# Kernel tuning notes

Hardware: AMD Instinct MI355X
Metric: run time of the kernel (lower is better)

The kernel has to match this reference:

```python
import jax, jax.numpy as jnp
import numpy as np
from jax import lax

NEG = -1e30  # effective -inf in fp32, safe under logaddexp
BLANK = 0


def setup_inputs() -> dict:
    key = jax.random.key(0)
    k1, k2, k3, k4 = jax.random.split(key, 4)
    B, T, V, S = 64, 2000, 128, 100
    logits = jax.random.normal(k1, (B, T, V), dtype=jnp.float32)
    targets = jax.random.randint(k2, (B, S), 1, V)  # exclude blank=0
    logits_lengths = jax.random.randint(k3, (B,), T // 2, T + 1)
    targets_lengths = jax.random.randint(k4, (B,), S // 2, S + 1)
    return {"logits": logits, "targets": targets,
            "logits_lengths": logits_lengths, "targets_lengths": targets_lengths}


def _ctc_neg_log_lik(log_probs, targets, in_lens, tgt_lens):
    # log_probs: [B, T, V] log-softmax; targets: [B, S]; lengths: [B]
    B, T, V = log_probs.shape
    S = targets.shape[1]
    L = 2 * S + 1  # extended label seq: blank, l1, blank, l2, ..., blank
    ext = jnp.full((B, L), BLANK, dtype=targets.dtype).at[:, 1::2].set(targets)
    # per-time emission log-prob of each extended-label slot: [B, T, L]
    lp_ext = jnp.take_along_axis(log_probs, ext[:, None, :], axis=2)
    # skip transition s-2 -> s allowed iff ext[s] != blank and ext[s] != ext[s-2]
    ext_m2 = jnp.pad(ext[:, :-2], ((0, 0), (2, 0)), constant_values=BLANK)
    skip = (ext != BLANK) & (ext != ext_m2)  # [B, L]

    alpha0 = jnp.full((B, L), NEG, dtype=log_probs.dtype)
    alpha0 = alpha0.at[:, 0].set(lp_ext[:, 0, 0])
    alpha0 = alpha0.at[:, 1].set(jnp.where(tgt_lens > 0, lp_ext[:, 0, 1], NEG))

    def step(alpha, xs):
        lp_t, t = xs  # lp_t: [B, L]
        a1 = jnp.pad(alpha[:, :-1], ((0, 0), (1, 0)), constant_values=NEG)
        a2 = jnp.where(skip,
                       jnp.pad(alpha[:, :-2], ((0, 0), (2, 0)), constant_values=NEG),
                       NEG)
        new = jnp.logaddexp(jnp.logaddexp(alpha, a1), a2) + lp_t
        # freeze alpha once past each utterance's length
        alpha = jnp.where((t < in_lens)[:, None], new, alpha)
        return alpha, None

    xs = (jnp.moveaxis(lp_ext, 1, 0)[1:], jnp.arange(1, T))
    alpha_T, _ = lax.scan(step, alpha0, xs)

    idx = 2 * tgt_lens  # final blank slot
    last_blank = jnp.take_along_axis(alpha_T, idx[:, None], axis=1)[:, 0]
    last_label = jnp.take_along_axis(alpha_T, jnp.maximum(idx - 1, 0)[:, None], axis=1)[:, 0]
    last_label = jnp.where(tgt_lens > 0, last_label, NEG)
    return -jnp.logaddexp(last_blank, last_label)  # [B]


def reference(logits, targets, logits_lengths, targets_lengths):
    log_probs = jax.nn.log_softmax(logits, axis=2)
    loss = _ctc_neg_log_lik(log_probs, targets, logits_lengths, targets_lengths)
    return loss.sum()  # reduce=True
```

## Files before the change

### kernel.cpp

```cpp
#include <hip/hip_runtime.h>
#include <hip/hip_fp16.h>
#include <math.h>

#define BB 64
#define TT 2000
#define VV 128
#define SS 100
#define NP 1000
#define PRB 448
#define LN2D 0.6931471805599453

__device__ __forceinline__ float wave_sum_f32(float v) {
    int t;
    t = __builtin_amdgcn_update_dpp(0, __float_as_int(v), 0x111, 0xF, 0xF, true);  v += __int_as_float(t);
    t = __builtin_amdgcn_update_dpp(0, __float_as_int(v), 0x112, 0xF, 0xF, true);  v += __int_as_float(t);
    t = __builtin_amdgcn_update_dpp(0, __float_as_int(v), 0x114, 0xF, 0xF, true);  v += __int_as_float(t);
    t = __builtin_amdgcn_update_dpp(0, __float_as_int(v), 0x118, 0xF, 0xF, true);  v += __int_as_float(t);
    t = __builtin_amdgcn_update_dpp(0, __float_as_int(v), 0x142, 0xA, 0xF, false); v += __int_as_float(t);
    t = __builtin_amdgcn_update_dpp(0, __float_as_int(v), 0x143, 0xC, 0xF, false); v += __int_as_float(t);
    return __int_as_float(__builtin_amdgcn_readlane(__float_as_int(v), 63));
}

__device__ __forceinline__ void half_sums_f32(float v, float* sA, float* sB) {
    int t;
    t = __builtin_amdgcn_update_dpp(0, __float_as_int(v), 0x111, 0xF, 0xF, true);  v += __int_as_float(t);
    t = __builtin_amdgcn_update_dpp(0, __float_as_int(v), 0x112, 0xF, 0xF, true);  v += __int_as_float(t);
    t = __builtin_amdgcn_update_dpp(0, __float_as_int(v), 0x114, 0xF, 0xF, true);  v += __int_as_float(t);
    t = __builtin_amdgcn_update_dpp(0, __float_as_int(v), 0x118, 0xF, 0xF, true);  v += __int_as_float(t);
    t = __builtin_amdgcn_update_dpp(0, __float_as_int(v), 0x142, 0xA, 0xF, false); v += __int_as_float(t);
    *sA = __int_as_float(__builtin_amdgcn_readlane(__float_as_int(v), 31));
    *sB = __int_as_float(__builtin_amdgcn_readlane(__float_as_int(v), 63));
}

__global__ __launch_bounds__(256) void ctc_k1(
    const float* __restrict__ logits, const int* __restrict__ targets,
    ushort* __restrict__ pe2, float* __restrict__ logSb)
{
    const int wv = threadIdx.x >> 6, lane = threadIdx.x & 63;
    const int gp = blockIdx.x * 4 + wv;
    const int b = gp / NP, p = gp - b * NP;
    const int tA = 2 * p + 1, tB = 2 * p + 2;
    const bool vB = (tB < TT);

    const int trow = (lane < 32) ? tA : (vB ? tB : tA);
    float4 x4 = reinterpret_cast<const float4*>(logits + ((size_t)b * TT + trow) * VV)[lane & 31];

    float e0 = __expf(x4.x), e1 = __expf(x4.y);
    float e2 = __expf(x4.z), e3 = __expf(x4.w);
    float sa, sb;
    half_sums_f32((e0 + e1) + (e2 + e3), &sa, &sb);

    __shared__ float sm[4][2][VV];
    {
        float4 ev; ev.x = e0; ev.y = e1; ev.z = e2; ev.w = e3;
        *reinterpret_cast<float4*>(&sm[wv][lane >> 5][(lane & 31) * 4]) = ev;
    }

    int tg0 = 0, tg1 = 0;
    if (lane < 50) {
        int2 tg = reinterpret_cast<const int2*>(targets)[b * (SS / 2) + lane];
        tg0 = tg.x; tg1 = tg.y;
    }
    const float qiA = 1.0f / sm[wv][0][0];
    const float qiB = 1.0f / sm[wv][1][0];
    float q1a = 0.f, q3a = 0.f, q1b = 0.f, q3b = 0.f;
    if (lane < 50) {
        q1a = fminf(sm[wv][0][tg0] * qiA, 65504.f);
        q3a = fminf(sm[wv][0][tg1] * qiA, 65504.f);
        if (vB) {
            q1b = fminf(sm[wv][1][tg0] * qiB, 65504.f);
            q3b = fminf(sm[wv][1][tg1] * qiB, 65504.f);
        }
    }
    if (lane < 56) {
        ushort4 w;
        w.x = __half_as_ushort(__float2half_rn(q1a));
        w.y = __half_as_ushort(__float2half_rn(q3a));
        w.z = __half_as_ushort(__float2half_rn(q1b));
        w.w = __half_as_ushort(__float2half_rn(q3b));
        *reinterpret_cast<ushort4*>((char*)pe2 + ((size_t)b * NP + p) * PRB + lane * 8) = w;
    }
    if (lane == 0) {
        float xB0 = __int_as_float(__builtin_amdgcn_readlane(__float_as_int(x4.x), 32));
        logSb[b * TT + tA] = __logf(sa) - x4.x;
        if (vB) logSb[b * TT + tB] = __logf(sb) - xB0;
    }
}

union H4 { uint2 u; __half h[4]; };

__device__ __forceinline__ double dpp_shr1_f64(double x) {
    long long bl = __double_as_longlong(x);
    int lo = (int)bl, hi = (int)(bl >> 32);
    lo = __builtin_amdgcn_update_dpp(0, lo, 0x138, 0xF, 0xF, true);
    hi = __builtin_amdgcn_update_dpp(0, hi, 0x138, 0xF, 0xF, true);
    return __longlong_as_double((long long)(((unsigned long long)(unsigned)hi << 32) | (unsigned)lo));
}

__device__ __forceinline__ double dpp_shl1_f64(double x) {
    long long bl = __double_as_longlong(x);
    int lo = (int)bl, hi = (int)(bl >> 32);
    lo = __builtin_amdgcn_update_dpp(0, lo, 0x130, 0xF, 0xF, true);
    hi = __builtin_amdgcn_update_dpp(0, hi, 0x130, 0xF, 0xF, true);
    return __longlong_as_double((long long)(((unsigned long long)(unsigned)hi << 32) | (unsigned)lo));
}

__device__ __forceinline__ int wave_max_i32(int v) {
    int t;
    t = __builtin_amdgcn_update_dpp(0, v, 0x111, 0xF, 0xF, true); v = v > t ? v : t;
    t = __builtin_amdgcn_update_dpp(0, v, 0x112, 0xF, 0xF, true); v = v > t ? v : t;
    t = __builtin_amdgcn_update_dpp(0, v, 0x114, 0xF, 0xF, true); v = v > t ? v : t;
    t = __builtin_amdgcn_update_dpp(0, v, 0x118, 0xF, 0xF, true); v = v > t ? v : t;
    t = __builtin_amdgcn_update_dpp(v, v, 0x142, 0xA, 0xF, false); v = v > t ? v : t;
    t = __builtin_amdgcn_update_dpp(v, v, 0x143, 0xC, 0xF, false); v = v > t ? v : t;
    return __builtin_amdgcn_readlane(v, 63);
}

#define FSTEP(Q1, Q3) do {                                   \
    double am1 = dpp_shr1_f64(a3);                           \
    double t23 = a2 + a3;                                    \
    double n3 = fma(sk3, a1, t23) * (Q3);                    \
    double t01 = a0 + a1;                                    \
    double n1 = fma(sk1, am1, t01) * (Q1);                   \
    double n0 = a0 + am1;                                    \
    double n2 = a1 + a2;                                     \
    a0 = n0; a1 = n1; a2 = n2; a3 = n3;                      \
} while (0)

#define BSTEP(Q1, Q3) do {                                   \
    double bp0 = dpp_shl1_f64(a0);                           \
    double bp1 = dpp_shl1_f64(a1);                           \
    double t12 = a1 + a2;                                    \
    double c1 = fma(sk3, a3, t12) * (Q1);                    \
    double c0 = a0 + a1;                                     \
    double t30 = a3 + bp0;                                   \
    double c3 = fma(skB, bp1, t30) * (Q3);                   \
    double c2 = a2 + a3;                                     \
    a0 = c0; a1 = c1; a2 = c2; a3 = c3;                      \
} while (0)

#define RENORM() do {                                        \
    int h0 = (int)(__double_as_longlong(a0) >> 32);          \
    int h1 = (int)(__double_as_longlong(a1) >> 32);          \
    int h2 = (int)(__double_as_longlong(a2) >> 32);          \
    int h3 = (int)(__double_as_longlong(a3) >> 32);          \
    int m01 = h0 > h1 ? h0 : h1;                             \
    int m23 = h2 > h3 ? h2 : h3;                             \
    int mm  = wave_max_i32(m01 > m23 ? m01 : m23);           \
    int ex  = (mm >> 20) & 0x7FF;                            \
    int exc = ex > 0 ? ex : 1;                               \
    double f = __longlong_as_double((long long)(2046 - exc) << 52); \
    a0 *= f; a1 *= f; a2 *= f; a3 *= f;                      \
    Epow += exc - 1023;                                      \
} while (0)

#define CVT4(H, Q1A, Q3A, Q1B, Q3B) do {                     \
    Q1A = (double)__half2float((H).h[0]);                    \
    Q3A = (double)__half2float((H).h[1]);                    \
    Q1B = (double)__half2float((H).h[2]);                    \
    Q3B = (double)__half2float((H).h[3]); } while (0)

__global__ __launch_bounds__(128) void ctc_k2(
    const float* __restrict__ logits, const ushort* __restrict__ pe2,
    const float* __restrict__ logSb, const int* __restrict__ targets,
    const int* __restrict__ in_lens, const int* __restrict__ tgt_lens,
    float* __restrict__ out)
{
    const int b    = blockIdx.x;
    const int tid  = threadIdx.x;
    const int wv   = tid >> 6;
    const int lane = tid & 63;
    const int n    = in_lens[b];
    const int tl   = tgt_lens[b];

    const int P  = (13 * (n - 2)) / 50;
    const int pL = (n - 2) >> 1;

    __shared__ double SA[256];
    __shared__ double SC[256];
    __shared__ double sred[2];
    __shared__ int    sE[2];

    int tg0 = 0, tg1 = 0, tgm1 = 0, tg2 = 0;
    if (lane < 50) {
        int2 tg = reinterpret_cast<const int2*>(targets)[b * (SS / 2) + lane];
        tg0 = tg.x; tg1 = tg.y;
    }
    if (lane >= 1 && lane <= 50) tgm1 = targets[b * SS + 2 * lane - 1];
    if (lane <= 48) tg2 = targets[b * SS + 2 * lane + 2];
    const double sk1 = (tg0 != tgm1) ? 1.0 : 0.0;
    const double sk3 = (tg1 != tg0)  ? 1.0 : 0.0;
    const double skB = (tg2 != tg1)  ? 1.0 : 0.0;

    const int cl = (lane < 51) ? lane : 50;
    const char* PBbase = (const char*)pe2 + (size_t)b * NP * PRB + (size_t)cl * 8;

    double a0 = 0.0, a1 = 0.0, a2 = 0.0, a3 = 0.0;
    int Epow = 0;
    double lsb0 = 0.0;
    uint2 buf[16];

    if (wv == 0) {
        float2 x0 = reinterpret_cast<const float2*>(logits + (size_t)b * TT * VV)[lane];
        float e00 = __expf(x0.x), e01 = __expf(x0.y);
        float s0v = wave_sum_f32(e00 + e01);
        float qb0 = __shfl(e00, 0);
        int ext1 = targets[b * SS];
        float qn = __shfl((ext1 & 1) ? e01 : e00, ext1 >> 1);
        if (lane == 0) {
            a0 = 1.0;
            if (tl > 0) a1 = (double)qn / (double)qb0;
            lsb0 = (double)__logf(s0v) - (double)x0.x;
        }

        #pragma unroll
        for (int d = 0; d < 16; ++d)
            buf[d] = *reinterpret_cast<const uint2*>(PBbase + (size_t)d * PRB);
        const char* Pc = PBbase + (size_t)16 * PRB;
        double c1A, c3A, c1B, c3B, n1A, n3A, n1B, n3B;
        { H4 h0; h0.u = buf[0]; CVT4(h0, c1A, c3A, c1B, c3B); }
        const int nfull = P >> 4, rem = P & 15;
        for (int c = 0; c < nfull; ++c) {
            #pragma unroll
            for (int d = 0; d < 16; ++d) {
                H4 hn; hn.u = buf[(d + 1) & 15];
                buf[d] = *reinterpret_cast<const uint2*>(Pc + (size_t)d * PRB);
                CVT4(hn, n1A, n3A, n1B, n3B);
                FSTEP(c1A, c3A);
                FSTEP(c1B, c3B);
                c1A = n1A; c3A = n3A; c1B = n1B; c3B = n3B;
            }
            RENORM();
            Pc += (size_t)16 * PRB;
        }
        #pragma unroll
        for (int d = 0; d < 16; ++d) {
            if (d < rem) {
                H4 h; h.u = buf[d];
                double q1A, q3A, q1B, q3B; CVT4(h, q1A, q3A, q1B, q3B);
                FSTEP(q1A, q3A);
                FSTEP(q1B, q3B);
            }
        }
        RENORM();
        SA[4 * lane + 0] = a0; SA[4 * lane + 1] = a1;
        SA[4 * lane + 2] = a2; SA[4 * lane + 3] = a3;
        if (lane == 0) sE[0] = Epow;
    } else {
        H4 hi; hi.u = *reinterpret_cast<const uint2*>(PBbase + (size_t)pL * PRB);
        const bool nOdd = (n & 1);
        double q1i = (double)__half2float(nOdd ? hi.h[2] : hi.h[0]);
        double q3i = (double)__half2float(nOdd ? hi.h[3] : hi.h[1]);
        const int s2 = 2 * tl, s1 = 2 * tl - 1;
        a0 = (4 * lane     == s2) ? 1.0 : 0.0;
        a1 = (4 * lane + 1 == s1) ? q1i : 0.0;
        a2 = (4 * lane + 2 == s2) ? 1.0 : 0.0;
        a3 = (4 * lane + 3 == s1) ? q3i : 0.0;
        if (nOdd) {
            double q1 = (double)__half2float(hi.h[0]);
            double q3 = (double)__half2float(hi.h[1]);
            BSTEP(q1, q3);
        }

        const int NB = pL - P;
        #pragma unroll
        for (int d = 0; d < 16; ++d)
            buf[d] = *reinterpret_cast<const uint2*>(PBbase + (size_t)(pL - 1 - d) * PRB);
        const char* Pc = PBbase + (size_t)(pL - 1 - 16) * PRB;
        double c1A, c3A, c1B, c3B, n1A, n3A, n1B, n3B;
        { H4 h0; h0.u = buf[0]; CVT4(h0, c1A, c3A, c1B, c3B); }
        const int nfull = NB >> 4, rem = NB & 15;
        for (int c = 0; c < nfull; ++c) {
            #pragma unroll
            for (int d = 0; d < 16; ++d) {
                H4 hn; hn.u = buf[(d + 1) & 15];
                buf[d] = *reinterpret_cast<const uint2*>(Pc - (size_t)d * PRB);
                CVT4(hn, n1A, n3A, n1B, n3B);
                BSTEP(c1B, c3B);
                BSTEP(c1A, c3A);
                c1A = n1A; c3A = n3A; c1B = n1B; c3B = n3B;
            }
            RENORM();
            Pc -= (size_t)16 * PRB;
        }
        #pragma unroll
        for (int d = 0; d < 16; ++d) {
            if (d < rem) {
                H4 h; h.u = buf[d];
                double q1A, q3A, q1B, q3B; CVT4(h, q1A, q3A, q1B, q3B);
                BSTEP(q1B, q3B);
                BSTEP(q1A, q3A);
            }
        }
        RENORM();
        {
            double bp0 = dpp_shl1_f64(a0);
            double bp1 = dpp_shl1_f64(a1);
            double c0 = a0 + a1;
            double c1 = fma(sk3, a3, a1 + a2);
            double c2 = a2 + a3;
            double c3 = fma(skB, bp1, a3 + bp0);
            SC[4 * lane + 0] = c0; SC[4 * lane + 1] = c1;
            SC[4 * lane + 2] = c2; SC[4 * lane + 3] = c3;
        }
        if (lane == 0) sE[1] = Epow;
    }

    double cb = 0.0;
    for (int t = 1 + tid; t < n; t += 128) cb += (double)logSb[b * TT + t];
    #pragma unroll
    for (int off = 32; off; off >>= 1) cb += __shfl_xor(cb, off);
    if (lane == 0) sred[wv] = cb;

    __syncthreads();

    if (wv == 0) {
        double d0 = SA[4 * lane + 0] * SC[4 * lane + 0]
                  + SA[4 * lane + 1] * SC[4 * lane + 1]
                  + SA[4 * lane + 2] * SC[4 * lane + 2]
                  + SA[4 * lane + 3] * SC[4 * lane + 3];
        #pragma unroll
        for (int off = 32; off; off >>= 1) d0 += __shfl_xor(d0, off);
        if (lane == 0) {
            double dot = d0;
            int extraE = 0;
            long long bits = __double_as_longlong(dot);
            int be = (int)((bits >> 52) & 0x7FF);
            if (be == 0) {
                dot *= 0x1.0p+512;
                bits = __double_as_longlong(dot);
                be = (int)((bits >> 52) & 0x7FF);
                extraE = -512;
            }
            double mant = __longlong_as_double((bits & 0xFFFFFFFFFFFFFLL) | 0x3FF0000000000000LL);
            double logdot = ((double)(be - 1023 + extraE + sE[0] + sE[1])) * LN2D
                          + (double)__logf((float)mant);
            double loss = (sred[0] + sred[1] + lsb0) - logdot;
            atomicAdd(out, (float)loss);
        }
    }
}

extern "C" void kernel_launch(void* const* d_in, const int* in_sizes, int n_in,
                              void* d_out, int out_size, void* d_ws, size_t ws_size,
                              hipStream_t stream)
{
    const float* logits  = (const float*)d_in[0];
    const int* targets   = (const int*)d_in[1];
    const int* in_lens   = (const int*)d_in[2];
    const int* tgt_lens  = (const int*)d_in[3];
    float* out = (float*)d_out;

    ushort* pe2 = (ushort*)d_ws;
    float* logSb = (float*)((char*)d_ws + (size_t)BB * NP * PRB);

    hipMemsetAsync(d_out, 0, sizeof(float), stream);
    ctc_k1<<<BB * NP / 4, 256, 0, stream>>>(logits, targets, pe2, logSb);
    ctc_k2<<<BB, 128, 0, stream>>>(logits, pe2, logSb, targets, in_lens, tgt_lens, out);
}
```

Before: 65.87 us.

## Interleave forward and backward CTC recursions in one wave, skip padded steps

The second kernel now runs the forward and backward alpha/beta recursions interleaved inside a single 64-lane wave instead of on two separate waves. This gives each wave two independent dependency chains to hide FP64 latency and removes the shared-memory exchange and block barrier. The split point moves from about 26% forward to an even half. The first kernel now returns early for time pairs past each utterance's length and zeroes the output itself, which replaces the memset launch. The risk is that the single wave's serial chain gets longer, and that zeroing the output from block 0 depends on kernel ordering.

New measurement: 105.7 us. +60.4%, slower.

```diff
diff --git a/kernel.cpp b/kernel.cpp
--- a/kernel.cpp
+++ b/kernel.cpp
@@ -34,11 +34,15 @@
 
 __global__ __launch_bounds__(256) void ctc_k1(
     const float* __restrict__ logits, const int* __restrict__ targets,
-    ushort* __restrict__ pe2, float* __restrict__ logSb)
+    const int* __restrict__ in_lens, ushort* __restrict__ pe2,
+    float* __restrict__ logSb, float* __restrict__ out)
 {
+    if (blockIdx.x == 0 && threadIdx.x == 0) out[0] = 0.f;
     const int wv = threadIdx.x >> 6, lane = threadIdx.x & 63;
     const int gp = blockIdx.x * 4 + wv;
     const int b = gp / NP, p = gp - b * NP;
+    const int n = in_lens[b];
+    if (p > ((n - 2) >> 1)) return;
     const int tA = 2 * p + 1, tB = 2 * p + 2;
     const bool vB = (tB < TT);
 
@@ -128,30 +132,30 @@
 } while (0)
 
 #define BSTEP(Q1, Q3) do {                                   \
-    double bp0 = dpp_shl1_f64(a0);                           \
-    double bp1 = dpp_shl1_f64(a1);                           \
-    double t12 = a1 + a2;                                    \
-    double c1 = fma(sk3, a3, t12) * (Q1);                    \
-    double c0 = a0 + a1;                                     \
-    double t30 = a3 + bp0;                                   \
+    double bp0 = dpp_shl1_f64(b0);                           \
+    double bp1 = dpp_shl1_f64(b1);                           \
+    double t12 = b1 + b2;                                    \
+    double c1 = fma(sk3, b3, t12) * (Q1);                    \
+    double c0 = b0 + b1;                                     \
+    double t30 = b3 + bp0;                                   \
     double c3 = fma(skB, bp1, t30) * (Q3);                   \
-    double c2 = a2 + a3;                                     \
-    a0 = c0; a1 = c1; a2 = c2; a3 = c3;                      \
+    double c2 = b2 + b3;                                     \
+    b0 = c0; b1 = c1; b2 = c2; b3 = c3;                      \
 } while (0)
 
-#define RENORM() do {                                        \
-    int h0 = (int)(__double_as_longlong(a0) >> 32);          \
-    int h1 = (int)(__double_as_longlong(a1) >> 32);          \
-    int h2 = (int)(__double_as_longlong(a2) >> 32);          \
-    int h3 = (int)(__double_as_longlong(a3) >> 32);          \
+#define RENORM4(X0, X1, X2, X3, EP) do {                     \
+    int h0 = (int)(__double_as_longlong(X0) >> 32);          \
+    int h1 = (int)(__double_as_longlong(X1) >> 32);          \
+    int h2 = (int)(__double_as_longlong(X2) >> 32);          \
+    int h3 = (int)(__double_as_longlong(X3) >> 32);          \
     int m01 = h0 > h1 ? h0 : h1;                             \
     int m23 = h2 > h3 ? h2 : h3;                             \
     int mm  = wave_max_i32(m01 > m23 ? m01 : m23);           \
     int ex  = (mm >> 20) & 0x7FF;                            \
     int exc = ex > 0 ? ex : 1;                               \
     double f = __longlong_as_double((long long)(2046 - exc) << 52); \
-    a0 *= f; a1 *= f; a2 *= f; a3 *= f;                      \
-    Epow += exc - 1023;                                      \
+    X0 *= f; X1 *= f; X2 *= f; X3 *= f;                      \
+    EP += exc - 1023;                                        \
 } while (0)
 
 #define CVT4(H, Q1A, Q3A, Q1B, Q3B) do {                     \
@@ -160,26 +164,20 @@
     Q1B = (double)__half2float((H).h[2]);                    \
     Q3B = (double)__half2float((H).h[3]); } while (0)
 
-__global__ __launch_bounds__(128) void ctc_k2(
+__global__ __launch_bounds__(64) void ctc_k2(
     const float* __restrict__ logits, const ushort* __restrict__ pe2,
     const float* __restrict__ logSb, const int* __restrict__ targets,
     const int* __restrict__ in_lens, const int* __restrict__ tgt_lens,
     float* __restrict__ out)
 {
     const int b    = blockIdx.x;
-    const int tid  = threadIdx.x;
-    const int wv   = tid >> 6;
-    const int lane = tid & 63;
+    const int lane = threadIdx.x;
     const int n    = in_lens[b];
     const int tl   = tgt_lens[b];
 
-    const int P  = (13 * (n - 2)) / 50;
     const int pL = (n - 2) >> 1;
-
-    __shared__ double SA[256];
-    __shared__ double SC[256];
-    __shared__ double sred[2];
-    __shared__ int    sE[2];
+    const int P  = (pL + 1) >> 1;
+    const int NB = pL - P;
 
     int tg0 = 0, tg1 = 0, tgm1 = 0, tg2 = 0;
     if (lane < 50) {
@@ -196,11 +194,8 @@
     const char* PBbase = (const char*)pe2 + (size_t)b * NP * PRB + (size_t)cl * 8;
 
     double a0 = 0.0, a1 = 0.0, a2 = 0.0, a3 = 0.0;
-    int Epow = 0;
     double lsb0 = 0.0;
-    uint2 buf[16];
-
-    if (wv == 0) {
+    {
         float2 x0 = reinterpret_cast<const float2*>(logits + (size_t)b * TT * VV)[lane];
         float e00 = __expf(x0.x), e01 = __expf(x0.y);
         float s0v = wave_sum_f32(e00 + e01);
@@ -212,132 +207,111 @@
             if (tl > 0) a1 = (double)qn / (double)qb0;
             lsb0 = (double)__logf(s0v) - (double)x0.x;
         }
-
-        #pragma unroll
-        for (int d = 0; d < 16; ++d)
-            buf[d] = *reinterpret_cast<const uint2*>(PBbase + (size_t)d * PRB);
-        const char* Pc = PBbase + (size_t)16 * PRB;
-        double c1A, c3A, c1B, c3B, n1A, n3A, n1B, n3B;
-        { H4 h0; h0.u = buf[0]; CVT4(h0, c1A, c3A, c1B, c3B); }
-        const int nfull = P >> 4, rem = P & 15;
-        for (int c = 0; c < nfull; ++c) {
-            #pragma unroll
-            for (int d = 0; d < 16; ++d) {
-                H4 hn; hn.u = buf[(d + 1) & 15];
-                buf[d] = *reinterpret_cast<const uint2*>(Pc + (size_t)d * PRB);
-                CVT4(hn, n1A, n3A, n1B, n3B);
-                FSTEP(c1A, c3A);
-                FSTEP(c1B, c3B);
-                c1A = n1A; c3A = n3A; c1B = n1B; c3B = n3B;
-            }
-            RENORM();
-            Pc += (size_t)16 * PRB;
-        }
-        #pragma unroll
-        for (int d = 0; d < 16; ++d) {
-            if (d < rem) {
-                H4 h; h.u = buf[d];
-                double q1A, q3A, q1B, q3B; CVT4(h, q1A, q3A, q1B, q3B);
-                FSTEP(q1A, q3A);
-                FSTEP(q1B, q3B);
-            }
-        }
-        RENORM();
-        SA[4 * lane + 0] = a0; SA[4 * lane + 1] = a1;
-        SA[4 * lane + 2] = a2; SA[4 * lane + 3] = a3;
-        if (lane == 0) sE[0] = Epow;
-    } else {
+    }
+
+    double b0 = 0.0, b1 = 0.0, b2 = 0.0, b3 = 0.0;
+    {
         H4 hi; hi.u = *reinterpret_cast<const uint2*>(PBbase + (size_t)pL * PRB);
         const bool nOdd = (n & 1);
         double q1i = (double)__half2float(nOdd ? hi.h[2] : hi.h[0]);
         double q3i = (double)__half2float(nOdd ? hi.h[3] : hi.h[1]);
         const int s2 = 2 * tl, s1 = 2 * tl - 1;
-        a0 = (4 * lane     == s2) ? 1.0 : 0.0;
-        a1 = (4 * lane + 1 == s1) ? q1i : 0.0;
-        a2 = (4 * lane + 2 == s2) ? 1.0 : 0.0;
-        a3 = (4 * lane + 3 == s1) ? q3i : 0.0;
+        b0 = (4 * lane     == s2) ? 1.0 : 0.0;
+        b1 = (4 * lane + 1 == s1) ? q1i : 0.0;
+        b2 = (4 * lane + 2 == s2) ? 1.0 : 0.0;
+        b3 = (4 * lane + 3 == s1) ? q3i : 0.0;
         if (nOdd) {
             double q1 = (double)__half2float(hi.h[0]);
             double q3 = (double)__half2float(hi.h[1]);
             BSTEP(q1, q3);
         }
-
-        const int NB = pL - P;
-        #pragma unroll
-        for (int d = 0; d < 16; ++d)
-            buf[d] = *reinterpret_cast<const uint2*>(PBbase + (size_t)(pL - 1 - d) * PRB);
-        const char* Pc = PBbase + (size_t)(pL - 1 - 16) * PRB;
-        double c1A, c3A, c1B, c3B, n1A, n3A, n1B, n3B;
-        { H4 h0; h0.u = buf[0]; CVT4(h0, c1A, c3A, c1B, c3B); }
-        const int nfull = NB >> 4, rem = NB & 15;
-        for (int c = 0; c < nfull; ++c) {
-            #pragma unroll
-            for (int d = 0; d < 16; ++d) {
-                H4 hn; hn.u = buf[(d + 1) & 15];
-                buf[d] = *reinterpret_cast<const uint2*>(Pc - (size_t)d * PRB);
-                CVT4(hn, n1A, n3A, n1B, n3B);
-                BSTEP(c1B, c3B);
-                BSTEP(c1A, c3A);
-                c1A = n1A; c3A = n3A; c1B = n1B; c3B = n3B;
-            }
-            RENORM();
-            Pc -= (size_t)16 * PRB;
-        }
+    }
+
+    int EpowF = 0, EpowB = 0;
+
+    uint2 bf[16], bb[16];
+    #pragma unroll
+    for (int d = 0; d < 16; ++d) {
+        bf[d] = *reinterpret_cast<const uint2*>(PBbase + (size_t)d * PRB);
+        bb[d] = *reinterpret_cast<const uint2*>(PBbase + (size_t)(pL - 1 - d) * PRB);
+    }
+    const char* Pf = PBbase + (size_t)16 * PRB;
+    const char* Pb = PBbase + (size_t)(pL - 1 - 16) * PRB;
+
+    const int nfull = NB >> 4;
+    for (int c = 0; c < nfull; ++c) {
         #pragma unroll
         for (int d = 0; d < 16; ++d) {
-            if (d < rem) {
-                H4 h; h.u = buf[d];
-                double q1A, q3A, q1B, q3B; CVT4(h, q1A, q3A, q1B, q3B);
-                BSTEP(q1B, q3B);
-                BSTEP(q1A, q3A);
-            }
-        }
-        RENORM();
-        {
-            double bp0 = dpp_shl1_f64(a0);
-            double bp1 = dpp_shl1_f64(a1);
-            double c0 = a0 + a1;
-            double c1 = fma(sk3, a3, a1 + a2);
-            double c2 = a2 + a3;
-            double c3 = fma(skB, bp1, a3 + bp0);
-            SC[4 * lane + 0] = c0; SC[4 * lane + 1] = c1;
-            SC[4 * lane + 2] = c2; SC[4 * lane + 3] = c3;
-        }
-        if (lane == 0) sE[1] = Epow;
+            H4 hf; hf.u = bf[d]; bf[d] = *reinterpret_cast<const uint2*>(Pf + (size_t)d * PRB);
+            H4 hb; hb.u = bb[d]; bb[d] = *reinterpret_cast<const uint2*>(Pb - (size_t)d * PRB);
+            double f1A, f3A, f1B, f3B, g1A, g3A, g1B, g3B;
+            CVT4(hf, f1A, f3A, f1B, f3B);
+            CVT4(hb, g1A, g3A, g1B, g3B);
+            FSTEP(f1A, f3A);
+            BSTEP(g1B, g3B);
+            FSTEP(f1B, f3B);
+            BSTEP(g1A, g3A);
+        }
+        RENORM4(a0, a1, a2, a3, EpowF);
+        RENORM4(b0, b1, b2, b3, EpowB);
+        Pf += (size_t)16 * PRB;
+        Pb -= (size_t)16 * PRB;
+    }
+    const int remf = P  - 16 * nfull;
+    const int remb = NB - 16 * nfull;
+    #pragma unroll
+    for (int d = 0; d < 16; ++d) {
+        if (d < remf) {
+            H4 hf; hf.u = bf[d];
+            double f1A, f3A, f1B, f3B; CVT4(hf, f1A, f3A, f1B, f3B);
+            FSTEP(f1A, f3A);
+            FSTEP(f1B, f3B);
+        }
+        if (d < remb) {
+            H4 hb; hb.u = bb[d];
+            double g1A, g3A, g1B, g3B; CVT4(hb, g1A, g3A, g1B, g3B);
+            BSTEP(g1B, g3B);
+            BSTEP(g1A, g3A);
+        }
+    }
+    RENORM4(a0, a1, a2, a3, EpowF);
+    RENORM4(b0, b1, b2, b3, EpowB);
+
+    double c0, c1v, c2, c3v;
+    {
+        double bp0 = dpp_shl1_f64(b0);
+        double bp1 = dpp_shl1_f64(b1);
+        c0  = b0 + b1;
+        c1v = fma(sk3, b3, b1 + b2);
+        c2  = b2 + b3;
+        c3v = fma(skB, bp1, b3 + bp0);
     }
 
     double cb = 0.0;
-    for (int t = 1 + tid; t < n; t += 128) cb += (double)logSb[b * TT + t];
+    for (int t = 1 + lane; t < n; t += 64) cb += (double)logSb[b * TT + t];
+
+    double d0 = a0 * c0 + a1 * c1v + a2 * c2 + a3 * c3v;
     #pragma unroll
-    for (int off = 32; off; off >>= 1) cb += __shfl_xor(cb, off);
-    if (lane == 0) sred[wv] = cb;
-
-    __syncthreads();
-
-    if (wv == 0) {
-        double d0 = SA[4 * lane + 0] * SC[4 * lane + 0]
-                  + SA[4 * lane + 1] * SC[4 * lane + 1]
-                  + SA[4 * lane + 2] * SC[4 * lane + 2]
-                  + SA[4 * lane + 3] * SC[4 * lane + 3];
-        #pragma unroll
-        for (int off = 32; off; off >>= 1) d0 += __shfl_xor(d0, off);
-        if (lane == 0) {
-            double dot = d0;
-            int extraE = 0;
-            long long bits = __double_as_longlong(dot);
-            int be = (int)((bits >> 52) & 0x7FF);
-            if (be == 0) {
-                dot *= 0x1.0p+512;
-                bits = __double_as_longlong(dot);
-                be = (int)((bits >> 52) & 0x7FF);
-                extraE = -512;
-            }
-            double mant = __longlong_as_double((bits & 0xFFFFFFFFFFFFFLL) | 0x3FF0000000000000LL);
-            double logdot = ((double)(be - 1023 + extraE + sE[0] + sE[1])) * LN2D
-                          + (double)__logf((float)mant);
-            double loss = (sred[0] + sred[1] + lsb0) - logdot;
-            atomicAdd(out, (float)loss);
-        }
+    for (int off = 32; off; off >>= 1) {
+        d0 += __shfl_xor(d0, off);
+        cb += __shfl_xor(cb, off);
+    }
+    if (lane == 0) {
+        double dot = d0;
+        int extraE = 0;
+        long long bits = __double_as_longlong(dot);
+        int be = (int)((bits >> 52) & 0x7FF);
+        if (be == 0) {
+            dot *= 0x1.0p+512;
+            bits = __double_as_longlong(dot);
+            be = (int)((bits >> 52) & 0x7FF);
+            extraE = -512;
+        }
+        double mant = __longlong_as_double((bits & 0xFFFFFFFFFFFFFLL) | 0x3FF0000000000000LL);
+        double logdot = ((double)(be - 1023 + extraE + EpowF + EpowB)) * LN2D
+                      + (double)__logf((float)mant);
+        double loss = (cb + lsb0) - logdot;
+        atomicAdd(out, (float)loss);
     }
 }
 
@@ -354,7 +328,6 @@
     ushort* pe2 = (ushort*)d_ws;
     float* logSb = (float*)((char*)d_ws + (size_t)BB * NP * PRB);
 
-    hipMemsetAsync(d_out, 0, sizeof(float), stream);
-    ctc_k1<<<BB * NP / 4, 256, 0, stream>>>(logits, targets, pe2, logSb);
-    ctc_k2<<<BB, 128, 0, stream>>>(logits, pe2, logSb, targets, in_lens, tgt_lens, out);
-}
+    ctc_k1<<<BB * NP / 4, 256, 0, stream>>>(logits, targets, in_lens, pe2, logSb, out);
+    ctc_k2<<<BB, 64, 0, stream>>>(logits, pe2, logSb, targets, in_lens, tgt_lens, out);
+}
```
